# Optimization experiments

Hardware: AMD Instinct MI355X
Metric: run time of the kernel (lower is better)

Reference implementation:

```python
import jax, jax.numpy as jnp
import numpy as np

IMG = 512      # diffusion image side
CUT_SIZE = 224 # CLIP input resolution
CUTN = 64
CUT_POW = 1.0


def setup_inputs() -> dict:
    key = jax.random.key(0)
    k1, k2, k3, k4 = jax.random.split(key, 4)
    B, C, H, W = 4, 3, IMG, IMG
    x = jax.random.normal(k1, (B, C, H, W), dtype=jnp.float32)
    max_size = min(H, W)
    min_size = min(H, W, CUT_SIZE)
    # size = int(rand()**cut_pow * (max_size - min_size) + min_size)
    u = jax.random.uniform(k2, (CUTN,))
    sizes = ((u ** CUT_POW) * (max_size - min_size) + min_size).astype(jnp.int32)
    # offsets uniform in [0, side - size]
    offsetx = (jax.random.uniform(k3, (CUTN,)) * (W - sizes + 1).astype(jnp.float32)).astype(jnp.int32)
    offsety = (jax.random.uniform(k4, (CUTN,)) * (H - sizes + 1).astype(jnp.float32)).astype(jnp.int32)
    return {"x": x, "sizes": sizes, "offsetx": offsetx, "offsety": offsety, "cut_size": CUT_SIZE}


def _make_cutouts(x, sizes, offsetx, offsety, S):
    # Fused batched crop + bilinear resize (torch F.interpolate, align_corners=False).
    B, C, H, W = x.shape
    N = sizes.shape[0]
    sizes_f = sizes.astype(x.dtype)
    # source coords within the crop: (j + 0.5) * size/S - 0.5, clamped at 0
    grid = jnp.arange(S, dtype=x.dtype) + 0.5                      # [S]
    src = jnp.maximum(sizes_f[:, None] / S * grid[None, :] - 0.5, 0.0)  # [N,S]
    i0 = jnp.floor(src).astype(jnp.int32)
    frac = src - i0.astype(x.dtype)                                # [N,S]
    i0 = jnp.minimum(i0, sizes[:, None] - 1)
    i1 = jnp.minimum(i0 + 1, sizes[:, None] - 1)
    # global indices into the full image (crops are square: same grid for y and x)
    Y0 = (offsety[:, None] + i0)[:, :, None]  # [N,S,1]
    Y1 = (offsety[:, None] + i1)[:, :, None]
    X0 = (offsetx[:, None] + i0)[:, None, :]  # [N,1,S]
    X1 = (offsetx[:, None] + i1)[:, None, :]
    wy = frac[:, :, None]                      # [N,S,1]
    wx = frac[:, None, :]                      # [N,1,S]
    # four-corner gather: each is [B,C,N,S,S]
    v00 = x[:, :, Y0, X0]
    v01 = x[:, :, Y0, X1]
    v10 = x[:, :, Y1, X0]
    v11 = x[:, :, Y1, X1]
    out = (v00 * (1 - wy) * (1 - wx) + v01 * (1 - wy) * wx
           + v10 * wy * (1 - wx) + v11 * wy * wx)
    # torch.cat over cutouts -> cutout-major: [N*B, C, S, S]
    return out.transpose(2, 0, 1, 3, 4).reshape(N * B, C, S, S)


def reference(x, sizes, offsetx, offsety, cut_size):
    return _make_cutouts(x, sizes, offsetx, offsety, cut_size)
```

## Files before the change

### kernel.cpp

```cpp
#include <hip/hip_runtime.h>

constexpr int S  = 224;
constexpr int B  = 4;
constexpr int C  = 3;
constexpr int H  = 512;
constexpr int W  = 512;
constexpr int N  = 64;
constexpr int PLANES = B * C;
constexpr int HROWS  = S / 2;
constexpr int ROWS_PER_HP  = N * HROWS;
constexpr int ROWS_PER_XCD = 3 * ROWS_PER_HP;
constexpr int WPB    = 4;
constexpr int BLOCKS_PER_XCD = ROWS_PER_XCD / WPB;
constexpr int GRID   = 8 * BLOCKS_PER_XCD;

__device__ __forceinline__ void load_lds16(const float* g, float* l) {
    __builtin_amdgcn_global_load_lds(
        (const __attribute__((address_space(1))) void*)g,
        (__attribute__((address_space(3))) void*)l,
        16, 0, 0);
}

__global__ __launch_bounds__(256) void cutouts_kernel(
    const float* __restrict__ x,
    const int*   __restrict__ sizes,
    const int*   __restrict__ offx,
    const int*   __restrict__ offy,
    float*       __restrict__ out)
{
    __shared__ float lds[WPB][2][W];

    const int lane = threadIdx.x & 63;
    const int wv   = threadIdx.x >> 6;

    const int k     = blockIdx.x & 7;
    const int w_row = (blockIdx.x >> 3) * WPB + wv;
    const int hpsel = w_row / ROWS_PER_HP;
    const int rem   = w_row - hpsel * ROWS_PER_HP;
    const int n     = rem / HROWS;
    const int il    = rem - n * HROWS;
    const int hp    = k + (hpsel << 3);
    const int pi    = hp >> 1;
    const int i     = (hp & 1) * HROWS + il;

    const int   sz    = sizes[n];
    const float scale = (float)sz * (1.0f / (float)S);

    const float sy  = fmaxf(scale * ((float)i + 0.5f) - 0.5f, 0.0f);
    const float fiy = floorf(sy);
    const float fy  = sy - fiy;
    const int   iy0 = min((int)fiy, sz - 1);
    const int   iy1 = min(iy0 + 1, sz - 1);

    const float* plane = x + (size_t)pi * (H * W);
    const float* r0 = plane + (size_t)(offy[n] + iy0) * W;
    const float* r1 = plane + (size_t)(offy[n] + iy1) * W;

    load_lds16(r0 + lane * 4,       &lds[wv][0][0]);
    load_lds16(r0 + 256 + lane * 4, &lds[wv][0][256]);
    load_lds16(r1 + lane * 4,       &lds[wv][1][0]);
    load_lds16(r1 + 256 + lane * 4, &lds[wv][1][256]);

    asm volatile("s_waitcnt vmcnt(0)" ::: "memory");
    __syncthreads();

    const int ox = offx[n];
    const float* l0 = &lds[wv][0][0];
    const float* l1 = &lds[wv][1][0];
    float* orow = out + (size_t)(n * PLANES + pi) * (S * S) + (size_t)i * S;

    #pragma unroll
    for (int r = 0; r < 4; ++r) {
        const int px = r * 64 + lane;
        if (r < 3 || px < S) {
            const float sx  = fmaxf(scale * ((float)px + 0.5f) - 0.5f, 0.0f);
            const float fix = floorf(sx);
            const float fx  = sx - fix;
            const int   ix  = min((int)fix, sz - 1) + ox;

            const float v00 = l0[ix], v01 = l0[ix + 1];
            const float v10 = l1[ix], v11 = l1[ix + 1];

            const float top = v00 + (v01 - v00) * fx;
            const float bot = v10 + (v11 - v10) * fx;
            orow[px] = top + (bot - top) * fy;
        }
    }
}

extern "C" void kernel_launch(void* const* d_in, const int* in_sizes, int n_in,
                              void* d_out, int out_size, void* d_ws, size_t ws_size,
                              hipStream_t stream) {
    const float* x     = (const float*)d_in[0];
    const int*   sizes = (const int*)d_in[1];
    const int*   offx  = (const int*)d_in[2];
    const int*   offy  = (const int*)d_in[3];
    float* out = (float*)d_out;

    cutouts_kernel<<<GRID, 256, 0, stream>>>(x, sizes, offx, offy, out);
}
```

Baseline: 47.50 us.

## Process two output rows per wave with overlapped LDS staging

Each wavefront now handles a pair of output rows, issuing the global-to-LDS loads for both rows up front. It then waits on a partial vmcnt before computing the first row, so the second row's loads overlap with the first row's compute and stores. This halves the grid size and doubles the LDS per block (32KB), which can reduce occupancy. The __syncthreads is removed because each wave uses its own LDS slice. The second vmcnt(4) wait relies on the first row's stores being counted in vmcnt.

```diff
diff --git a/kernel.cpp b/kernel.cpp
--- a/kernel.cpp
+++ b/kernel.cpp
@@ -8,10 +8,10 @@
 constexpr int N  = 64;
 constexpr int PLANES = B * C;
 constexpr int HROWS  = S / 2;
-constexpr int ROWS_PER_HP  = N * HROWS;
-constexpr int ROWS_PER_XCD = 3 * ROWS_PER_HP;
+constexpr int PAIRS_PER_HP  = N * (HROWS / 2);
+constexpr int PAIRS_PER_XCD = 3 * PAIRS_PER_HP;
 constexpr int WPB    = 4;
-constexpr int BLOCKS_PER_XCD = ROWS_PER_XCD / WPB;
+constexpr int BLOCKS_PER_XCD = PAIRS_PER_XCD / WPB;
 constexpr int GRID   = 8 * BLOCKS_PER_XCD;
 
 __device__ __forceinline__ void load_lds16(const float* g, float* l) {
@@ -21,54 +21,26 @@
         16, 0, 0);
 }
 
-__global__ __launch_bounds__(256) void cutouts_kernel(
-    const float* __restrict__ x,
-    const int*   __restrict__ sizes,
-    const int*   __restrict__ offx,
-    const int*   __restrict__ offy,
-    float*       __restrict__ out)
-{
-    __shared__ float lds[WPB][2][W];
-
-    const int lane = threadIdx.x & 63;
-    const int wv   = threadIdx.x >> 6;
-
-    const int k     = blockIdx.x & 7;
-    const int w_row = (blockIdx.x >> 3) * WPB + wv;
-    const int hpsel = w_row / ROWS_PER_HP;
-    const int rem   = w_row - hpsel * ROWS_PER_HP;
-    const int n     = rem / HROWS;
-    const int il    = rem - n * HROWS;
-    const int hp    = k + (hpsel << 3);
-    const int pi    = hp >> 1;
-    const int i     = (hp & 1) * HROWS + il;
-
-    const int   sz    = sizes[n];
-    const float scale = (float)sz * (1.0f / (float)S);
-
+__device__ __forceinline__ void stage_row(const float* plane, int oy, int i,
+                                          float scale, int sz, int lane,
+                                          float* buf, float& fy_out) {
     const float sy  = fmaxf(scale * ((float)i + 0.5f) - 0.5f, 0.0f);
     const float fiy = floorf(sy);
-    const float fy  = sy - fiy;
-    const int   iy0 = min((int)fiy, sz - 1);
-    const int   iy1 = min(iy0 + 1, sz - 1);
+    fy_out = sy - fiy;
+    const int iy0 = min((int)fiy, sz - 1);
+    const int iy1 = min(iy0 + 1, sz - 1);
+    const float* r0 = plane + (size_t)(oy + iy0) * W;
+    const float* r1 = plane + (size_t)(oy + iy1) * W;
+    load_lds16(r0 + lane * 4,       buf);
+    load_lds16(r0 + 256 + lane * 4, buf + 256);
+    load_lds16(r1 + lane * 4,       buf + W);
+    load_lds16(r1 + 256 + lane * 4, buf + W + 256);
+}
 
-    const float* plane = x + (size_t)pi * (H * W);
-    const float* r0 = plane + (size_t)(offy[n] + iy0) * W;
-    const float* r1 = plane + (size_t)(offy[n] + iy1) * W;
-
-    load_lds16(r0 + lane * 4,       &lds[wv][0][0]);
-    load_lds16(r0 + 256 + lane * 4, &lds[wv][0][256]);
-    load_lds16(r1 + lane * 4,       &lds[wv][1][0]);
-    load_lds16(r1 + 256 + lane * 4, &lds[wv][1][256]);
-
-    asm volatile("s_waitcnt vmcnt(0)" ::: "memory");
-    __syncthreads();
-
-    const int ox = offx[n];
-    const float* l0 = &lds[wv][0][0];
-    const float* l1 = &lds[wv][1][0];
-    float* orow = out + (size_t)(n * PLANES + pi) * (S * S) + (size_t)i * S;
-
+__device__ __forceinline__ void compute_row(const float* buf, float fy, float scale,
+                                            int sz, int ox, int lane, float* orow) {
+    const float* l0 = buf;
+    const float* l1 = buf + W;
     #pragma unroll
     for (int r = 0; r < 4; ++r) {
         const int px = r * 64 + lane;
@@ -77,15 +49,57 @@
             const float fix = floorf(sx);
             const float fx  = sx - fix;
             const int   ix  = min((int)fix, sz - 1) + ox;
-
             const float v00 = l0[ix], v01 = l0[ix + 1];
             const float v10 = l1[ix], v11 = l1[ix + 1];
-
             const float top = v00 + (v01 - v00) * fx;
             const float bot = v10 + (v11 - v10) * fx;
             orow[px] = top + (bot - top) * fy;
         }
     }
+}
+
+__global__ __launch_bounds__(256) void cutouts_kernel(
+    const float* __restrict__ x,
+    const int*   __restrict__ sizes,
+    const int*   __restrict__ offx,
+    const int*   __restrict__ offy,
+    float*       __restrict__ out)
+{
+    __shared__ float lds[WPB][2][2 * W];
+
+    const int lane = threadIdx.x & 63;
+    const int wv   = threadIdx.x >> 6;
+
+    const int k     = blockIdx.x & 7;
+    const int pair  = (blockIdx.x >> 3) * WPB + wv;
+    const int hpsel = pair / PAIRS_PER_HP;
+    const int rem   = pair - hpsel * PAIRS_PER_HP;
+    const int n     = rem / (HROWS / 2);
+    const int mp    = rem - n * (HROWS / 2);
+    const int hp    = k + (hpsel << 3);
+    const int pi    = hp >> 1;
+    const int i0    = (hp & 1) * HROWS + 2 * mp;
+    const int i1    = i0 + 1;
+
+    const int   sz    = sizes[n];
+    const float scale = (float)sz * (1.0f / (float)S);
+    const int   oy    = offy[n];
+    const int   ox    = offx[n];
+    const float* plane = x + (size_t)pi * (H * W);
+
+    float fy0, fy1;
+    stage_row(plane, oy, i0, scale, sz, lane, &lds[wv][0][0], fy0);
+    stage_row(plane, oy, i1, scale, sz, lane, &lds[wv][1][0], fy1);
+
+    float* obase = out + (size_t)(n * PLANES + pi) * (S * S);
+
+    asm volatile("s_waitcnt vmcnt(4)" ::: "memory");
+    __builtin_amdgcn_sched_barrier(0);
+    compute_row(&lds[wv][0][0], fy0, scale, sz, ox, lane, obase + (size_t)i0 * S);
+
+    asm volatile("s_waitcnt vmcnt(4)" ::: "memory");
+    __builtin_amdgcn_sched_barrier(0);
+    compute_row(&lds[wv][1][0], fy1, scale, sz, ox, lane, obase + (size_t)i1 * S);
 }
 
 extern "C" void kernel_launch(void* const* d_in, const int* in_sizes, int n_in,
```

Result: faster. 45.26 us (-4.7%).

## Stage 32-row image bands in LDS and serve many cutouts' rows from each band

Applied to the files above, without the earlier changes.

Replaces the one-wave-per-output-row scheme, which fetched two source rows from global memory per output row, with blocks that load a 33-row band of one image plane into LDS once. Each block then emits every output row of a group of four cutouts whose source rows fall in that band, found by inverting the resize mapping. This cuts redundant global reads of the same input rows across cutouts and rows. In exchange the blocks are larger (512 threads, about 68KB LDS), the work per block is uneven, and the row-range search adds some scalar work.

```diff
diff --git a/kernel.cpp b/kernel.cpp
--- a/kernel.cpp
+++ b/kernel.cpp
@@ -1,18 +1,18 @@
 #include <hip/hip_runtime.h>
 
-constexpr int S  = 224;
-constexpr int B  = 4;
-constexpr int C  = 3;
-constexpr int H  = 512;
-constexpr int W  = 512;
-constexpr int N  = 64;
-constexpr int PLANES = B * C;
-constexpr int HROWS  = S / 2;
-constexpr int ROWS_PER_HP  = N * HROWS;
-constexpr int ROWS_PER_XCD = 3 * ROWS_PER_HP;
-constexpr int WPB    = 4;
-constexpr int BLOCKS_PER_XCD = ROWS_PER_XCD / WPB;
-constexpr int GRID   = 8 * BLOCKS_PER_XCD;
+constexpr int S   = 224;
+constexpr int Wim = 512;
+constexpr int Him = 512;
+constexpr int PLANES = 12;
+constexpr int SB   = 32;
+constexpr int NBANDS = Him / SB;
+constexpr int NGRP = 4;
+constexpr int GROUPS = 64 / NGRP;
+constexpr int TILES = PLANES * NBANDS;
+constexpr int TPX   = TILES / 8;
+constexpr int LOCALS = TPX * GROUPS;
+constexpr int GRID   = 8 * LOCALS;
+constexpr int ROWPAD = Wim + 4;
 
 __device__ __forceinline__ void load_lds16(const float* g, float* l) {
     __builtin_amdgcn_global_load_lds(
@@ -21,69 +21,94 @@
         16, 0, 0);
 }
 
-__global__ __launch_bounds__(256) void cutouts_kernel(
+__device__ __forceinline__ int iy0_of(int i, float scale, int sz) {
+    const float sy = fmaxf(scale * ((float)i + 0.5f) - 0.5f, 0.0f);
+    return min((int)floorf(sy), sz - 1);
+}
+
+__device__ __forceinline__ int first_ge(float scale, int sz, int P) {
+    if (P <= 0) return 0;
+    if (P > sz - 1) return S;
+    float c = ((float)P + 0.5f) / scale - 0.5f;
+    int i = (int)ceilf(fminf(fmaxf(c, 0.0f), (float)S));
+    while (i > 0 && iy0_of(i - 1, scale, sz) >= P) --i;
+    while (i < S && iy0_of(i, scale, sz) < P) ++i;
+    return i;
+}
+
+__global__ __launch_bounds__(512) void cutouts_kernel(
     const float* __restrict__ x,
     const int*   __restrict__ sizes,
     const int*   __restrict__ offx,
     const int*   __restrict__ offy,
     float*       __restrict__ out)
 {
-    __shared__ float lds[WPB][2][W];
+    __shared__ float lds[SB + 1][ROWPAD];
 
     const int lane = threadIdx.x & 63;
     const int wv   = threadIdx.x >> 6;
 
-    const int k     = blockIdx.x & 7;
-    const int w_row = (blockIdx.x >> 3) * WPB + wv;
-    const int hpsel = w_row / ROWS_PER_HP;
-    const int rem   = w_row - hpsel * ROWS_PER_HP;
-    const int n     = rem / HROWS;
-    const int il    = rem - n * HROWS;
-    const int hp    = k + (hpsel << 3);
-    const int pi    = hp >> 1;
-    const int i     = (hp & 1) * HROWS + il;
+    const int xcd   = blockIdx.x & 7;
+    const int local = blockIdx.x >> 3;
+    const int g     = local / TPX;
+    const int tk    = local - g * TPX;
+    const int t     = xcd * TPX + tk;
+    const int pi    = t >> 4;
+    const int b     = t & (NBANDS - 1);
 
-    const int   sz    = sizes[n];
-    const float scale = (float)sz * (1.0f / (float)S);
+    if (threadIdx.x < (SB + 1) * 4)
+        lds[threadIdx.x >> 2][Wim + (threadIdx.x & 3)] = 0.0f;
 
-    const float sy  = fmaxf(scale * ((float)i + 0.5f) - 0.5f, 0.0f);
-    const float fiy = floorf(sy);
-    const float fy  = sy - fiy;
-    const int   iy0 = min((int)fiy, sz - 1);
-    const int   iy1 = min(iy0 + 1, sz - 1);
-
-    const float* plane = x + (size_t)pi * (H * W);
-    const float* r0 = plane + (size_t)(offy[n] + iy0) * W;
-    const float* r1 = plane + (size_t)(offy[n] + iy1) * W;
-
-    load_lds16(r0 + lane * 4,       &lds[wv][0][0]);
-    load_lds16(r0 + 256 + lane * 4, &lds[wv][0][256]);
-    load_lds16(r1 + lane * 4,       &lds[wv][1][0]);
-    load_lds16(r1 + 256 + lane * 4, &lds[wv][1][256]);
-
+    const float* plane = x + (size_t)pi * (Him * Wim);
+    for (int c = wv; c < (SB + 1) * 2; c += 8) {
+        const int row  = c >> 1, half = c & 1;
+        const int srow = min(SB * b + row, Him - 1);
+        load_lds16(plane + (size_t)srow * Wim + half * 256 + lane * 4,
+                   &lds[row][half * 256]);
+    }
     asm volatile("s_waitcnt vmcnt(0)" ::: "memory");
     __syncthreads();
 
-    const int ox = offx[n];
-    const float* l0 = &lds[wv][0][0];
-    const float* l1 = &lds[wv][1][0];
-    float* orow = out + (size_t)(n * PLANES + pi) * (S * S) + (size_t)i * S;
+    #pragma unroll
+    for (int nn = 0; nn < NGRP; ++nn) {
+        const int n  = g * NGRP + nn;
+        const int sz = sizes[n];
+        const int oy = offy[n];
+        const int ox = offx[n];
+        const float scale = (float)sz * (1.0f / (float)S);
 
-    #pragma unroll
-    for (int r = 0; r < 4; ++r) {
-        const int px = r * 64 + lane;
-        if (r < 3 || px < S) {
-            const float sx  = fmaxf(scale * ((float)px + 0.5f) - 0.5f, 0.0f);
-            const float fix = floorf(sx);
-            const float fx  = sx - fix;
-            const int   ix  = min((int)fix, sz - 1) + ox;
+        const int L = SB * b - oy;
+        const int R = L + SB;
+        const int i_lo = first_ge(scale, sz, L);
+        const int i_hi = first_ge(scale, sz, R);
 
-            const float v00 = l0[ix], v01 = l0[ix + 1];
-            const float v10 = l1[ix], v11 = l1[ix + 1];
+        float* oplane = out + (size_t)(n * PLANES + pi) * (S * S);
 
-            const float top = v00 + (v01 - v00) * fx;
-            const float bot = v10 + (v11 - v10) * fx;
-            orow[px] = top + (bot - top) * fy;
+        for (int i = i_lo + wv; i < i_hi; i += 8) {
+            const float sy  = fmaxf(scale * ((float)i + 0.5f) - 0.5f, 0.0f);
+            const float fiy = floorf(sy);
+            const float fy  = sy - fiy;
+            const int   iy0 = min((int)fiy, sz - 1);
+            const int   iy1 = min(iy0 + 1, sz - 1);
+            const float* l0 = &lds[iy0 - L][0];
+            const float* l1 = &lds[iy1 - L][0];
+            float* orow = oplane + (size_t)i * S;
+
+            #pragma unroll
+            for (int r = 0; r < 4; ++r) {
+                const int px = r * 64 + lane;
+                if (r < 3 || px < S) {
+                    const float sx  = fmaxf(scale * ((float)px + 0.5f) - 0.5f, 0.0f);
+                    const float fix = floorf(sx);
+                    const float fx  = sx - fix;
+                    const int   ix  = min((int)fix, sz - 1) + ox;
+                    const float v00 = l0[ix], v01 = l0[ix + 1];
+                    const float v10 = l1[ix], v11 = l1[ix + 1];
+                    const float top = v00 + (v01 - v00) * fx;
+                    const float bot = v10 + (v11 - v10) * fx;
+                    orow[px] = top + (bot - top) * fy;
+                }
+            }
         }
     }
 }
@@ -97,5 +122,5 @@
     const int*   offy  = (const int*)d_in[3];
     float* out = (float*)d_out;
 
-    cutouts_kernel<<<GRID, 256, 0, stream>>>(x, sizes, offx, offy, out);
+    cutouts_kernel<<<GRID, 512, 0, stream>>>(x, sizes, offx, offy, out);
 }
```

New measurement: 71.18 us. 1.5x slower.

## Replace LDS row staging with direct per-lane buffer_load_dwordx2 gathers

Applied to the files above, without the earlier changes.

Removes the shared-memory staging of two full 512-float source rows per wave and instead has each lane fetch its two horizontal neighbours from both rows with buffer_load_dwordx2 through a raw buffer resource. Edge clamping is reformulated so the left index is capped at size-2 and the weight absorbs the shift, which keeps each pair load in bounds and contiguous. This avoids loading unused parts of each row and drops the block barrier, at the cost of scattered, partly redundant 8-byte global reads that depend on cache hits, plus hardcoded resource descriptor bits and a 32-bit byte offset.

```diff
diff --git a/kernel.cpp b/kernel.cpp
--- a/kernel.cpp
+++ b/kernel.cpp
@@ -1,24 +1,33 @@
 #include <hip/hip_runtime.h>
+#include <stdint.h>
 
-constexpr int S  = 224;
-constexpr int B  = 4;
-constexpr int C  = 3;
-constexpr int H  = 512;
-constexpr int W  = 512;
-constexpr int N  = 64;
-constexpr int PLANES = B * C;
-constexpr int HROWS  = S / 2;
+constexpr int S   = 224;
+constexpr int Wim = 512;
+constexpr int Him = 512;
+constexpr int PLANES = 12;
+constexpr int N   = 64;
+constexpr int HROWS = S / 2;
 constexpr int ROWS_PER_HP  = N * HROWS;
 constexpr int ROWS_PER_XCD = 3 * ROWS_PER_HP;
-constexpr int WPB    = 4;
+constexpr int WPB = 4;
 constexpr int BLOCKS_PER_XCD = ROWS_PER_XCD / WPB;
-constexpr int GRID   = 8 * BLOCKS_PER_XCD;
+constexpr int GRID = 8 * BLOCKS_PER_XCD;
+constexpr uint32_t XBYTES = (uint32_t)PLANES * Him * Wim * 4u;
 
-__device__ __forceinline__ void load_lds16(const float* g, float* l) {
-    __builtin_amdgcn_global_load_lds(
-        (const __attribute__((address_space(1))) void*)g,
-        (__attribute__((address_space(3))) void*)l,
-        16, 0, 0);
+typedef float    f32x2   __attribute__((ext_vector_type(2)));
+typedef uint32_t srsrc_t __attribute__((ext_vector_type(4)));
+
+__device__ __forceinline__ f32x2 bload2_r0(srsrc_t srd, uint32_t voff) {
+    f32x2 d;
+    asm volatile("buffer_load_dwordx2 %0, %1, %2, 0 offen"
+                 : "=v"(d) : "v"(voff), "s"(srd) : "memory");
+    return d;
+}
+__device__ __forceinline__ f32x2 bload2_r1(srsrc_t srd, uint32_t voff) {
+    f32x2 d;
+    asm volatile("buffer_load_dwordx2 %0, %1, %2, 0 offen offset:2048"
+                 : "=v"(d) : "v"(voff), "s"(srd) : "memory");
+    return d;
 }
 
 __global__ __launch_bounds__(256) void cutouts_kernel(
@@ -28,8 +37,6 @@
     const int*   __restrict__ offy,
     float*       __restrict__ out)
 {
-    __shared__ float lds[WPB][2][W];
-
     const int lane = threadIdx.x & 63;
     const int wv   = threadIdx.x >> 6;
 
@@ -44,46 +51,53 @@
     const int i     = (hp & 1) * HROWS + il;
 
     const int   sz    = sizes[n];
-    const float scale = (float)sz * (1.0f / (float)S);
+    const float scale = (float)sz / (float)S;
+    const int   oy    = offy[n];
+    const int   ox    = offx[n];
 
     const float sy  = fmaxf(scale * ((float)i + 0.5f) - 0.5f, 0.0f);
     const float fiy = floorf(sy);
-    const float fy  = sy - fiy;
-    const int   iy0 = min((int)fiy, sz - 1);
-    const int   iy1 = min(iy0 + 1, sz - 1);
+    const int   iy0 = (int)fiy;
+    const int   ay  = min(iy0, sz - 2);
+    const float fy  = (sy - fiy) + (float)(iy0 - ay);
 
-    const float* plane = x + (size_t)pi * (H * W);
-    const float* r0 = plane + (size_t)(offy[n] + iy0) * W;
-    const float* r1 = plane + (size_t)(offy[n] + iy1) * W;
+    const uint32_t rowbase =
+        ((uint32_t)pi * (uint32_t)(Him * Wim) + (uint32_t)(oy + ay) * Wim + (uint32_t)ox) * 4u;
 
-    load_lds16(r0 + lane * 4,       &lds[wv][0][0]);
-    load_lds16(r0 + 256 + lane * 4, &lds[wv][0][256]);
-    load_lds16(r1 + lane * 4,       &lds[wv][1][0]);
-    load_lds16(r1 + 256 + lane * 4, &lds[wv][1][256]);
+    srsrc_t srd;
+    {
+        const uint64_t a = (uint64_t)(uintptr_t)x;
+        srd.x = (uint32_t)a;
+        srd.y = (uint32_t)(a >> 32);
+        srd.z = XBYTES;
+        srd.w = 0x00020000u;
+    }
 
+    float fxv[4];
+    f32x2 p0[4], p1[4];
+    #pragma unroll
+    for (int r = 0; r < 4; ++r) {
+        const int   px  = r * 64 + lane;
+        const float sx  = fmaxf(scale * ((float)px + 0.5f) - 0.5f, 0.0f);
+        const float fix = floorf(sx);
+        const int   ix0 = (int)fix;
+        const int   a   = min(ix0, sz - 2);
+        fxv[r] = (sx - fix) + (float)(ix0 - a);
+        const uint32_t voff = rowbase + (uint32_t)a * 4u;
+        p0[r] = bload2_r0(srd, voff);
+        p1[r] = bload2_r1(srd, voff);
+    }
     asm volatile("s_waitcnt vmcnt(0)" ::: "memory");
-    __syncthreads();
+    __builtin_amdgcn_sched_barrier(0);
 
-    const int ox = offx[n];
-    const float* l0 = &lds[wv][0][0];
-    const float* l1 = &lds[wv][1][0];
     float* orow = out + (size_t)(n * PLANES + pi) * (S * S) + (size_t)i * S;
-
     #pragma unroll
     for (int r = 0; r < 4; ++r) {
         const int px = r * 64 + lane;
-        if (r < 3 || px < S) {
-            const float sx  = fmaxf(scale * ((float)px + 0.5f) - 0.5f, 0.0f);
-            const float fix = floorf(sx);
-            const float fx  = sx - fix;
-            const int   ix  = min((int)fix, sz - 1) + ox;
-
-            const float v00 = l0[ix], v01 = l0[ix + 1];
-            const float v10 = l1[ix], v11 = l1[ix + 1];
-
-            const float top = v00 + (v01 - v00) * fx;
-            const float bot = v10 + (v11 - v10) * fx;
-            orow[px] = top + (bot - top) * fy;
+        if (r < 3 || lane < 32) {
+            const float h0 = p0[r].x + (p0[r].y - p0[r].x) * fxv[r];
+            const float h1 = p1[r].x + (p1[r].y - p1[r].x) * fxv[r];
+            orow[px] = h0 + (h1 - h0) * fy;
         }
     }
 }
```

Measured after the change: 58.67 us. 1.24x slower.
